# Kernel optimization log

Measured on AMD Instinct MI355X. Metric: run time of the kernel, lower is better.

## Reference

```python
import jax, jax.numpy as jnp
import numpy as np

G = 32        # group_num
PD = 8        # primary capsule dim
OC = 10       # output caps (classes)
OD = 16       # output dim
GS = 36       # group_size = primary spatial 6*6
N_ITERS = 3   # routing iterations


def conv2d(x, w, stride):
    return jax.lax.conv_general_dilated(
        x, w, window_strides=(stride, stride), padding='VALID',
        dimension_numbers=('NCHW', 'OIHW', 'NCHW'))


def squash(x):
    l2 = jnp.sum(x * x, axis=-1, keepdims=True)
    l = jnp.sqrt(l2)
    return x * (l2 / (1.0 + l2)) / (l + 1e-8)


def setup_inputs() -> dict:
    key = jax.random.key(0)
    ks = jax.random.split(key, 6)
    B = 256
    inp = jax.random.normal(ks[0], (B, 1, 28, 28), dtype=jnp.float32)
    W1 = jax.random.normal(ks[1], (256, 1, 9, 9), dtype=jnp.float32) * 0.05
    b1 = jnp.zeros((256,), dtype=jnp.float32)
    W2 = jax.random.normal(ks[2], (G * PD, 256, 9, 9), dtype=jnp.float32) * 0.01
    b2 = jnp.zeros((G * PD,), dtype=jnp.float32)
    Wcaps = jax.random.normal(ks[3], (G, GS, PD, OC * OD), dtype=jnp.float32) * 0.01
    b_route = jnp.zeros((G, 1, GS, OC), dtype=jnp.float32)
    return {'input': inp, 'W1': W1, 'b1': b1, 'W2': W2, 'b2': b2,
            'Wcaps': Wcaps, 'b_route': b_route}


def reference(input, W1, b1, W2, b2, Wcaps, b_route):
    B = input.shape[0]
    # conv1 + relu: (B,256,20,20)
    x = jax.nn.relu(conv2d(input, W1, 1) + b1[None, :, None, None])
    # primary caps conv: (B,256,6,6)
    y = conv2d(x, W2, 2) + b2[None, :, None, None]
    H = y.shape[2]
    # (B,G,PD,H,W) -> (B,G,H,W,PD) -> (B,G,GS,PD)
    y = y.reshape(B, G, PD, H, H).transpose(0, 1, 3, 4, 2).reshape(B, G, GS, PD)
    u = squash(y)
    # capsule predictions: (B,G,GS,OC,OD)
    up = jnp.einsum('bgsi,gsio->bgso', u, Wcaps).reshape(B, G, GS, OC, OD)
    # routing logits: (B,G,GS,OC)
    b = jnp.broadcast_to(jnp.transpose(b_route, (1, 0, 2, 3)), (B, G, GS, OC))
    v = None
    for r in range(N_ITERS):
        c = jax.nn.softmax(b, axis=3)                       # (B,G,GS,OC)
        s = jnp.einsum('bgso,bgsod->bgod', c, up)           # (B,G,OC,OD)
        v = squash(s)
        if r < N_ITERS - 1:
            b = b + jnp.einsum('bgsod,bgod->bgso', up, v)
    v = v.sum(axis=1)                                       # (B,OC,OD)
    probs = jnp.sqrt(jnp.sum(v * v, axis=2))                # (B,OC)
    return v, probs
```

## Files before the change

### kernel.cpp

```cpp
#include <hip/hip_runtime.h>
#include <math.h>


typedef float floatx4 __attribute__((ext_vector_type(4)));
typedef __bf16 bf16x8 __attribute__((ext_vector_type(8)));

#define XHI_OFF 0u
#define XLO_OFF 52428800u
#define WHI_OFF 104857600u
#define WLO_OFF 115867648u
#define Y2_OFF  126877696u
#define VP_OFF  136314880u
#define Y2_BYTES 9437184u

#define SL_IY   88
#define SL_IMG  1760
#define SL_PAR  7072
#define SL_TOT  14144

__device__ __forceinline__ void bf16split(float v, short& hs, short& ls) {
  unsigned u = __builtin_bit_cast(unsigned, v);
  unsigned r = (u + 0x7FFFu + ((u >> 16) & 1u)) & 0xFFFF0000u;
  hs = (short)(r >> 16);
  float lo = v - __builtin_bit_cast(float, r);
  unsigned u2 = __builtin_bit_cast(unsigned, lo);
  unsigned r2 = u2 + 0x7FFFu + ((u2 >> 16) & 1u);
  ls = (short)(r2 >> 16);
}

__global__ __launch_bounds__(320) void conv1_k(
    const float* __restrict__ inp, const float* __restrict__ W1,
    const float* __restrict__ b1, short* __restrict__ xhi,
    short* __restrict__ xlo) {
  __shared__ __align__(16) float img[784];
  __shared__ float wl[81 * 34];
  const int blk = blockIdx.x;
  const int b = blk >> 3;
  const int cbase = (blk & 7) * 32;
  const int t = threadIdx.x;

  const float4* src = (const float4*)(inp + b * 784);
  for (int idx = t; idx < 196; idx += 320) ((float4*)img)[idx] = src[idx];
  for (int idx = t; idx < 2592; idx += 320) {
    int c = idx / 81, tap = idx - c * 81;
    wl[tap * 34 + c] = W1[(cbase + c) * 81 + tap];
  }
  __syncthreads();

  const int oy = t >> 4;
  const int ct = t & 15;
  const int c0 = cbase + ct * 2;
  const float bias0 = b1[c0], bias1 = b1[c0 + 1];
  float acc0[20], acc1[20];
#pragma unroll
  for (int ox = 0; ox < 20; ox++) { acc0[ox] = bias0; acc1[ox] = bias1; }

#pragma unroll 1
  for (int i = 0; i < 9; i++) {
    float wr0[9], wr1[9];
#pragma unroll
    for (int j = 0; j < 9; j++) {
      float2 wv = *(const float2*)&wl[(i * 9 + j) * 34 + ct * 2];
      wr0[j] = wv.x; wr1[j] = wv.y;
    }
    float xr[28];
    const float4* rp = (const float4*)&img[(oy + i) * 28];
#pragma unroll
    for (int k = 0; k < 7; k++) {
      float4 v = rp[k];
      xr[4 * k] = v.x; xr[4 * k + 1] = v.y; xr[4 * k + 2] = v.z; xr[4 * k + 3] = v.w;
    }
#pragma unroll
    for (int j = 0; j < 9; j++)
#pragma unroll
      for (int ox = 0; ox < 20; ox++) {
        acc0[ox] = fmaf(xr[ox + j], wr0[j], acc0[ox]);
        acc1[ox] = fmaf(xr[ox + j], wr1[j], acc1[ox]);
      }
  }
  const long pbase = (long)(b * 400 + oy * 20) * 256 + c0;
#pragma unroll
  for (int ox = 0; ox < 20; ox++) {
    float v0 = fmaxf(acc0[ox], 0.f), v1 = fmaxf(acc1[ox], 0.f);
    short h0, l0, h1, l1;
    bf16split(v0, h0, l0);
    bf16split(v1, h1, l1);
    long a = pbase + (long)ox * 256;
    *(short2*)&xhi[a] = make_short2(h0, h1);
    *(short2*)&xlo[a] = make_short2(l0, l1);
  }
}

__global__ __launch_bounds__(256) void wtrans_k(
    const float* __restrict__ W2, short* __restrict__ whi,
    short* __restrict__ wlo) {
  const int idx = blockIdx.x * 256 + threadIdx.x;
  const int ics = idx & 7;
  const int oc = (idx >> 3) & 255;
  const int icg = (idx >> 11) & 31;
  const int tap = idx >> 16;
  short h = 0, l = 0;
  if (tap < 81) {
    const int ic = icg * 8 + ics;
    bf16split(W2[(oc * 256 + ic) * 81 + tap], h, l);
  }
  whi[idx] = h;
  wlo[idx] = l;
}

__global__ __launch_bounds__(256, 2) void conv2_k(
    const short* __restrict__ xhi, const short* __restrict__ xlo,
    const short* __restrict__ whi, const short* __restrict__ wlo,
    float* __restrict__ y2) {
  __shared__ __align__(16) short slabA[SL_TOT];

  const int blk = blockIdx.x;
  const int ks = blk & 15;
  const int mb = blk >> 4;
  const int b0 = mb * 4;
  const int t = threadIdx.x;
  const int lane = t & 63;
  const int q = lane >> 4;
  const int ln16 = lane & 15;
  const int wv = t >> 6;

  int combo[9];
#pragma unroll
  for (int mt = 0; mt < 9; mt++) {
    int row = mt * 16 + ln16;
    int im = row / 36;
    int pos = row - im * 36;
    int oy = pos / 6, ox = pos - oy * 6;
    combo[mt] = im * SL_IMG + oy * (2 * SL_IY) + ox * 8;
  }

  floatx4 acc[9][4];
#pragma unroll
  for (int mt = 0; mt < 9; mt++)
#pragma unroll
    for (int nt = 0; nt < 4; nt++) acc[mt][nt] = (floatx4)0.f;

#pragma unroll 1
  for (int icg = 0; icg < 2; icg++) {
    const int icgG = ks * 2 + icg;
    const long icoff = (long)icgG * 8;
    const long wb0 = ((long)icgG * 256 + wv * 64 + ln16) * 8 + (long)q * 65536;

    __syncthreads();
    for (int idx = t; idx < 1600; idx += 256) {
      int im = idx / 400, p = idx - im * 400;
      int iy = p / 20, ix = p - iy * 20;
      int dst = (ix & 1) * SL_PAR + im * SL_IMG + iy * SL_IY + (ix >> 1) * 8;
      *(uint4*)&slabA[dst] =
          *(const uint4*)&xhi[((long)(b0 + im) * 400 + p) * 256 + icoff];
    }
    __syncthreads();

    {
      bf16x8 cbh[4];
#pragma unroll
      for (int nt = 0; nt < 4; nt++) cbh[nt] = *(const bf16x8*)&whi[wb0 + nt * 128];
#pragma unroll 1
      for (int kst = 0; kst < 21; kst++) {
        const int t0n = (kst < 20) ? (kst + 1) * 4 : 80;
        bf16x8 nbh[4], cbl[4];
#pragma unroll
        for (int nt = 0; nt < 4; nt++) {
          nbh[nt] = *(const bf16x8*)&whi[wb0 + (long)t0n * 65536 + nt * 128];
          cbl[nt] = *(const bf16x8*)&wlo[wb0 + (long)(kst * 4) * 65536 + nt * 128];
        }
        const int tap = kst * 4 + q;
        const int i = tap / 9, j = tap - i * 9;
        const int aoff = (j & 1) * SL_PAR + i * SL_IY + (j >> 1) * 8;
#pragma unroll
        for (int bb = 0; bb < 3; bb++) {
          bf16x8 av[3];
#pragma unroll
          for (int m3 = 0; m3 < 3; m3++)
            av[m3] = *(const bf16x8*)&slabA[aoff + combo[bb * 3 + m3]];
#pragma unroll
          for (int nt = 0; nt < 4; nt++)
#pragma unroll
            for (int m3 = 0; m3 < 3; m3++)
              acc[bb * 3 + m3][nt] = __builtin_amdgcn_mfma_f32_16x16x32_bf16(
                  av[m3], cbh[nt], acc[bb * 3 + m3][nt], 0, 0, 0);
#pragma unroll
          for (int nt = 0; nt < 4; nt++)
#pragma unroll
            for (int m3 = 0; m3 < 3; m3++)
              acc[bb * 3 + m3][nt] = __builtin_amdgcn_mfma_f32_16x16x32_bf16(
                  av[m3], cbl[nt], acc[bb * 3 + m3][nt], 0, 0, 0);
        }
#pragma unroll
        for (int nt = 0; nt < 4; nt++) cbh[nt] = nbh[nt];
      }
    }

    __syncthreads();
    for (int idx = t; idx < 1600; idx += 256) {
      int im = idx / 400, p = idx - im * 400;
      int iy = p / 20, ix = p - iy * 20;
      int dst = (ix & 1) * SL_PAR + im * SL_IMG + iy * SL_IY + (ix >> 1) * 8;
      *(uint4*)&slabA[dst] =
          *(const uint4*)&xlo[((long)(b0 + im) * 400 + p) * 256 + icoff];
    }
    __syncthreads();

    {
      bf16x8 cbh[4];
#pragma unroll
      for (int nt = 0; nt < 4; nt++) cbh[nt] = *(const bf16x8*)&whi[wb0 + nt * 128];
#pragma unroll 1
      for (int kst = 0; kst < 21; kst++) {
        const int t0n = (kst < 20) ? (kst + 1) * 4 : 80;
        bf16x8 nbh[4];
#pragma unroll
        for (int nt = 0; nt < 4; nt++)
          nbh[nt] = *(const bf16x8*)&whi[wb0 + (long)t0n * 65536 + nt * 128];
        const int tap = kst * 4 + q;
        const int i = tap / 9, j = tap - i * 9;
        const int aoff = (j & 1) * SL_PAR + i * SL_IY + (j >> 1) * 8;
#pragma unroll
        for (int bb = 0; bb < 3; bb++) {
          bf16x8 av[3];
#pragma unroll
          for (int m3 = 0; m3 < 3; m3++)
            av[m3] = *(const bf16x8*)&slabA[aoff + combo[bb * 3 + m3]];
#pragma unroll
          for (int nt = 0; nt < 4; nt++)
#pragma unroll
            for (int m3 = 0; m3 < 3; m3++)
              acc[bb * 3 + m3][nt] = __builtin_amdgcn_mfma_f32_16x16x32_bf16(
                  av[m3], cbh[nt], acc[bb * 3 + m3][nt], 0, 0, 0);
        }
#pragma unroll
        for (int nt = 0; nt < 4; nt++) cbh[nt] = nbh[nt];
      }
    }
  }

#pragma unroll
  for (int mt = 0; mt < 9; mt++)
#pragma unroll
    for (int nt = 0; nt < 4; nt++) {
      int oc = wv * 64 + nt * 16 + ln16;
      int rowb = mb * 144 + mt * 16 + q * 4;
#pragma unroll
      for (int r = 0; r < 4; r++)
        atomicAdd(&y2[(long)(rowb + r) * 256 + oc], acc[mt][nt][r]);
    }
}

__global__ __launch_bounds__(256) void caps_k(
    const float* __restrict__ y2, const float* __restrict__ b2,
    const float* __restrict__ Wcaps, const float* __restrict__ b_route,
    float* __restrict__ vpart) {
  __shared__ float u[288];
  __shared__ float usc[36];
  __shared__ float up[5760];
  __shared__ float bl[360];
  __shared__ float cl[360];
  __shared__ float sv[160];
  __shared__ float vv[160];
  __shared__ float scale[10];
  const int blk = blockIdx.x;
  const int g = blk & 31, b = blk >> 5;
  const int t = threadIdx.x;

  for (int idx = t; idx < 288; idx += 256) {
    int s = idx >> 3, d = idx & 7;
    u[idx] = y2[((long)b * 36 + s) * 256 + g * 8 + d] + b2[g * 8 + d];
  }
  for (int idx = t; idx < 360; idx += 256) bl[idx] = b_route[g * 360 + idx];
  __syncthreads();
  if (t < 36) {
    float l2 = 0.f;
#pragma unroll
    for (int d = 0; d < 8; d++) { float v = u[t * 8 + d]; l2 = fmaf(v, v, l2); }
    float l = sqrtf(l2);
    usc[t] = (l2 / (1.f + l2)) / (l + 1e-8f);
  }
  __syncthreads();
  for (int idx = t; idx < 288; idx += 256) u[idx] *= usc[idx >> 3];
  __syncthreads();
  for (int idx = t; idx < 5760; idx += 256) {
    int s = idx / 160, k = idx - s * 160;
    const float* wp = Wcaps + (g * 36 + s) * 8 * 160 + k;
    float a = 0.f;
#pragma unroll
    for (int d = 0; d < 8; d++) a = fmaf(u[s * 8 + d], wp[d * 160], a);
    up[idx] = a;
  }
  __syncthreads();

  for (int r = 0; r < 3; r++) {
    if (t < 36) {
      float m = bl[t * 10];
#pragma unroll
      for (int oc = 1; oc < 10; oc++) m = fmaxf(m, bl[t * 10 + oc]);
      float e[10]; float sum = 0.f;
#pragma unroll
      for (int oc = 0; oc < 10; oc++) { e[oc] = expf(bl[t * 10 + oc] - m); sum += e[oc]; }
      float inv = 1.f / sum;
#pragma unroll
      for (int oc = 0; oc < 10; oc++) cl[t * 10 + oc] = e[oc] * inv;
    }
    __syncthreads();
    if (t < 160) {
      const int oc = t >> 4;
      float a = 0.f;
#pragma unroll 1
      for (int s = 0; s < 36; s++) a = fmaf(cl[s * 10 + oc], up[s * 160 + t], a);
      sv[t] = a;
    }
    __syncthreads();
    if (t < 10) {
      float l2 = 0.f;
#pragma unroll
      for (int od = 0; od < 16; od++) { float v = sv[t * 16 + od]; l2 = fmaf(v, v, l2); }
      scale[t] = (l2 / (1.f + l2)) / (sqrtf(l2) + 1e-8f);
    }
    __syncthreads();
    if (t < 160) vv[t] = sv[t] * scale[t >> 4];
    __syncthreads();
    if (r < 2) {
      for (int idx = t; idx < 360; idx += 256) {
        int s = idx / 10, oc = idx - s * 10;
        float a = 0.f;
#pragma unroll
        for (int od = 0; od < 16; od++)
          a = fmaf(up[s * 160 + oc * 16 + od], vv[oc * 16 + od], a);
        bl[idx] += a;
      }
      __syncthreads();
    }
  }
  if (t < 160) vpart[(b * 32 + g) * 160 + t] = vv[t];
}

__global__ __launch_bounds__(192) void final_k(
    const float* __restrict__ vpart, float* __restrict__ out) {
  __shared__ float v[160];
  const int b = blockIdx.x, t = threadIdx.x;
  if (t < 160) {
    float a = 0.f;
#pragma unroll 1
    for (int g = 0; g < 32; g++) a += vpart[(b * 32 + g) * 160 + t];
    v[t] = a;
    out[b * 160 + t] = a;
  }
  __syncthreads();
  if (t < 10) {
    float l2 = 0.f;
#pragma unroll
    for (int od = 0; od < 16; od++) { float x = v[t * 16 + od]; l2 = fmaf(x, x, l2); }
    out[40960 + b * 10 + t] = sqrtf(l2);
  }
}

extern "C" void kernel_launch(void* const* d_in, const int* in_sizes, int n_in,
                              void* d_out, int out_size, void* d_ws, size_t ws_size,
                              hipStream_t stream) {
  const float* inp     = (const float*)d_in[0];
  const float* W1      = (const float*)d_in[1];
  const float* b1      = (const float*)d_in[2];
  const float* W2      = (const float*)d_in[3];
  const float* b2      = (const float*)d_in[4];
  const float* Wcaps   = (const float*)d_in[5];
  const float* b_route = (const float*)d_in[6];
  float* out = (float*)d_out;
  char* ws = (char*)d_ws;

  short* xhi = (short*)(ws + XHI_OFF);
  short* xlo = (short*)(ws + XLO_OFF);
  short* whi = (short*)(ws + WHI_OFF);
  short* wlo = (short*)(ws + WLO_OFF);
  float* y2  = (float*)(ws + Y2_OFF);
  float* vp  = (float*)(ws + VP_OFF);

  hipMemsetAsync(y2, 0, Y2_BYTES, stream);
  conv1_k <<<2048, 320, 0, stream>>>(inp, W1, b1, xhi, xlo);
  wtrans_k<<<21504, 256, 0, stream>>>(W2, whi, wlo);
  conv2_k <<<1024, 256, 0, stream>>>(xhi, xlo, whi, wlo, y2);
  caps_k  <<<8192, 256, 0, stream>>>(y2, b2, Wcaps, b_route, vp);
  final_k <<<256, 192, 0, stream>>>(vp, out);
}
```

Measured before the change: 579.6 us.

## Fuse hi/lo conv2 passes, halve K-split, and shrink caps blocks to one wave

```diff
diff --git a/kernel.cpp b/kernel.cpp
--- a/kernel.cpp
+++ b/kernel.cpp
@@ -4,6 +4,7 @@
 
 typedef float floatx4 __attribute__((ext_vector_type(4)));
 typedef __bf16 bf16x8 __attribute__((ext_vector_type(8)));
+typedef unsigned uintx4 __attribute__((ext_vector_type(4)));
 
 #define XHI_OFF 0u
 #define XLO_OFF 52428800u
@@ -112,11 +113,12 @@
     const short* __restrict__ xhi, const short* __restrict__ xlo,
     const short* __restrict__ whi, const short* __restrict__ wlo,
     float* __restrict__ y2) {
-  __shared__ __align__(16) short slabA[SL_TOT];
+  __shared__ __align__(16) short slabH[SL_TOT];
+  __shared__ __align__(16) short slabL[SL_TOT];
 
   const int blk = blockIdx.x;
-  const int ks = blk & 15;
-  const int mb = blk >> 4;
+  const int ks = blk & 7;
+  const int mb = blk >> 3;
   const int b0 = mb * 4;
   const int t = threadIdx.x;
   const int lane = t & 63;
@@ -141,8 +143,8 @@
     for (int nt = 0; nt < 4; nt++) acc[mt][nt] = (floatx4)0.f;
 
 #pragma unroll 1
-  for (int icg = 0; icg < 2; icg++) {
-    const int icgG = ks * 2 + icg;
+  for (int icg = 0; icg < 4; icg++) {
+    const int icgG = ks * 4 + icg;
     const long icoff = (long)icgG * 8;
     const long wb0 = ((long)icgG * 256 + wv * 64 + ln16) * 8 + (long)q * 65536;
 
@@ -151,91 +153,61 @@
       int im = idx / 400, p = idx - im * 400;
       int iy = p / 20, ix = p - iy * 20;
       int dst = (ix & 1) * SL_PAR + im * SL_IMG + iy * SL_IY + (ix >> 1) * 8;
-      *(uint4*)&slabA[dst] =
-          *(const uint4*)&xhi[((long)(b0 + im) * 400 + p) * 256 + icoff];
-    }
-    __syncthreads();
-
-    {
-      bf16x8 cbh[4];
-#pragma unroll
-      for (int nt = 0; nt < 4; nt++) cbh[nt] = *(const bf16x8*)&whi[wb0 + nt * 128];
+      const long src = ((long)(b0 + im) * 400 + p) * 256 + icoff;
+      uintx4 vh = __builtin_nontemporal_load((const uintx4*)&xhi[src]);
+      uintx4 vl = __builtin_nontemporal_load((const uintx4*)&xlo[src]);
+      *(uintx4*)&slabH[dst] = vh;
+      *(uintx4*)&slabL[dst] = vl;
+    }
+    __syncthreads();
+
+    bf16x8 cbh[4], cbl[4];
+#pragma unroll
+    for (int nt = 0; nt < 4; nt++) {
+      cbh[nt] = *(const bf16x8*)&whi[wb0 + nt * 128];
+      cbl[nt] = *(const bf16x8*)&wlo[wb0 + nt * 128];
+    }
 #pragma unroll 1
-      for (int kst = 0; kst < 21; kst++) {
-        const int t0n = (kst < 20) ? (kst + 1) * 4 : 80;
-        bf16x8 nbh[4], cbl[4];
-#pragma unroll
-        for (int nt = 0; nt < 4; nt++) {
-          nbh[nt] = *(const bf16x8*)&whi[wb0 + (long)t0n * 65536 + nt * 128];
-          cbl[nt] = *(const bf16x8*)&wlo[wb0 + (long)(kst * 4) * 65536 + nt * 128];
+    for (int kst = 0; kst < 21; kst++) {
+      const int t0n = (kst < 20) ? (kst + 1) * 4 : 80;
+      bf16x8 nbh[4], nbl[4];
+#pragma unroll
+      for (int nt = 0; nt < 4; nt++) {
+        nbh[nt] = *(const bf16x8*)&whi[wb0 + (long)t0n * 65536 + nt * 128];
+        nbl[nt] = *(const bf16x8*)&wlo[wb0 + (long)t0n * 65536 + nt * 128];
+      }
+      const int tap = kst * 4 + q;
+      const int i = tap / 9, j = tap - i * 9;
+      const int aoff = (j & 1) * SL_PAR + i * SL_IY + (j >> 1) * 8;
+#pragma unroll
+      for (int bb = 0; bb < 3; bb++) {
+        bf16x8 ah[3], al[3];
+#pragma unroll
+        for (int m3 = 0; m3 < 3; m3++) {
+          ah[m3] = *(const bf16x8*)&slabH[aoff + combo[bb * 3 + m3]];
+          al[m3] = *(const bf16x8*)&slabL[aoff + combo[bb * 3 + m3]];
         }
-        const int tap = kst * 4 + q;
-        const int i = tap / 9, j = tap - i * 9;
-        const int aoff = (j & 1) * SL_PAR + i * SL_IY + (j >> 1) * 8;
-#pragma unroll
-        for (int bb = 0; bb < 3; bb++) {
-          bf16x8 av[3];
+#pragma unroll
+        for (int nt = 0; nt < 4; nt++)
 #pragma unroll
           for (int m3 = 0; m3 < 3; m3++)
-            av[m3] = *(const bf16x8*)&slabA[aoff + combo[bb * 3 + m3]];
-#pragma unroll
-          for (int nt = 0; nt < 4; nt++)
-#pragma unroll
-            for (int m3 = 0; m3 < 3; m3++)
-              acc[bb * 3 + m3][nt] = __builtin_amdgcn_mfma_f32_16x16x32_bf16(
-                  av[m3], cbh[nt], acc[bb * 3 + m3][nt], 0, 0, 0);
-#pragma unroll
-          for (int nt = 0; nt < 4; nt++)
-#pragma unroll
-            for (int m3 = 0; m3 < 3; m3++)
-              acc[bb * 3 + m3][nt] = __builtin_amdgcn_mfma_f32_16x16x32_bf16(
-                  av[m3], cbl[nt], acc[bb * 3 + m3][nt], 0, 0, 0);
-        }
-#pragma unroll
-        for (int nt = 0; nt < 4; nt++) cbh[nt] = nbh[nt];
+            acc[bb * 3 + m3][nt] = __builtin_amdgcn_mfma_f32_16x16x32_bf16(
+                ah[m3], cbh[nt], acc[bb * 3 + m3][nt], 0, 0, 0);
+#pragma unroll
+        for (int nt = 0; nt < 4; nt++)
+#pragma unroll
+          for (int m3 = 0; m3 < 3; m3++)
+            acc[bb * 3 + m3][nt] = __builtin_amdgcn_mfma_f32_16x16x32_bf16(
+                ah[m3], cbl[nt], acc[bb * 3 + m3][nt], 0, 0, 0);
+#pragma unroll
+        for (int nt = 0; nt < 4; nt++)
+#pragma unroll
+          for (int m3 = 0; m3 < 3; m3++)
+            acc[bb * 3 + m3][nt] = __builtin_amdgcn_mfma_f32_16x16x32_bf16(
+                al[m3], cbh[nt], acc[bb * 3 + m3][nt], 0, 0, 0);
       }
-    }
-
-    __syncthreads();
-    for (int idx = t; idx < 1600; idx += 256) {
-      int im = idx / 400, p = idx - im * 400;
-      int iy = p / 20, ix = p - iy * 20;
-      int dst = (ix & 1) * SL_PAR + im * SL_IMG + iy * SL_IY + (ix >> 1) * 8;
-      *(uint4*)&slabA[dst] =
-          *(const uint4*)&xlo[((long)(b0 + im) * 400 + p) * 256 + icoff];
-    }
-    __syncthreads();
-
-    {
-      bf16x8 cbh[4];
-#pragma unroll
-      for (int nt = 0; nt < 4; nt++) cbh[nt] = *(const bf16x8*)&whi[wb0 + nt * 128];
-#pragma unroll 1
-      for (int kst = 0; kst < 21; kst++) {
-        const int t0n = (kst < 20) ? (kst + 1) * 4 : 80;
-        bf16x8 nbh[4];
-#pragma unroll
-        for (int nt = 0; nt < 4; nt++)
-          nbh[nt] = *(const bf16x8*)&whi[wb0 + (long)t0n * 65536 + nt * 128];
-        const int tap = kst * 4 + q;
-        const int i = tap / 9, j = tap - i * 9;
-        const int aoff = (j & 1) * SL_PAR + i * SL_IY + (j >> 1) * 8;
-#pragma unroll
-        for (int bb = 0; bb < 3; bb++) {
-          bf16x8 av[3];
-#pragma unroll
-          for (int m3 = 0; m3 < 3; m3++)
-            av[m3] = *(const bf16x8*)&slabA[aoff + combo[bb * 3 + m3]];
-#pragma unroll
-          for (int nt = 0; nt < 4; nt++)
-#pragma unroll
-            for (int m3 = 0; m3 < 3; m3++)
-              acc[bb * 3 + m3][nt] = __builtin_amdgcn_mfma_f32_16x16x32_bf16(
-                  av[m3], cbh[nt], acc[bb * 3 + m3][nt], 0, 0, 0);
-        }
-#pragma unroll
-        for (int nt = 0; nt < 4; nt++) cbh[nt] = nbh[nt];
-      }
+#pragma unroll
+      for (int nt = 0; nt < 4; nt++) { cbh[nt] = nbh[nt]; cbl[nt] = nbl[nt]; }
     }
   }
 
@@ -251,7 +223,7 @@
     }
 }
 
-__global__ __launch_bounds__(256) void caps_k(
+__global__ __launch_bounds__(64) void caps_k(
     const float* __restrict__ y2, const float* __restrict__ b2,
     const float* __restrict__ Wcaps, const float* __restrict__ b_route,
     float* __restrict__ vpart) {
@@ -267,11 +239,11 @@
   const int g = blk & 31, b = blk >> 5;
   const int t = threadIdx.x;
 
-  for (int idx = t; idx < 288; idx += 256) {
+  for (int idx = t; idx < 288; idx += 64) {
     int s = idx >> 3, d = idx & 7;
     u[idx] = y2[((long)b * 36 + s) * 256 + g * 8 + d] + b2[g * 8 + d];
   }
-  for (int idx = t; idx < 360; idx += 256) bl[idx] = b_route[g * 360 + idx];
+  for (int idx = t; idx < 360; idx += 64) bl[idx] = b_route[g * 360 + idx];
   __syncthreads();
   if (t < 36) {
     float l2 = 0.f;
@@ -281,9 +253,9 @@
     usc[t] = (l2 / (1.f + l2)) / (l + 1e-8f);
   }
   __syncthreads();
-  for (int idx = t; idx < 288; idx += 256) u[idx] *= usc[idx >> 3];
-  __syncthreads();
-  for (int idx = t; idx < 5760; idx += 256) {
+  for (int idx = t; idx < 288; idx += 64) u[idx] *= usc[idx >> 3];
+  __syncthreads();
+  for (int idx = t; idx < 5760; idx += 64) {
     int s = idx / 160, k = idx - s * 160;
     const float* wp = Wcaps + (g * 36 + s) * 8 * 160 + k;
     float a = 0.f;
@@ -306,12 +278,12 @@
       for (int oc = 0; oc < 10; oc++) cl[t * 10 + oc] = e[oc] * inv;
     }
     __syncthreads();
-    if (t < 160) {
-      const int oc = t >> 4;
+    for (int idx = t; idx < 160; idx += 64) {
+      const int oc = idx >> 4;
       float a = 0.f;
-#pragma unroll 1
-      for (int s = 0; s < 36; s++) a = fmaf(cl[s * 10 + oc], up[s * 160 + t], a);
-      sv[t] = a;
+#pragma unroll 4
+      for (int s = 0; s < 36; s++) a = fmaf(cl[s * 10 + oc], up[s * 160 + idx], a);
+      sv[idx] = a;
     }
     __syncthreads();
     if (t < 10) {
@@ -321,10 +293,10 @@
       scale[t] = (l2 / (1.f + l2)) / (sqrtf(l2) + 1e-8f);
     }
     __syncthreads();
-    if (t < 160) vv[t] = sv[t] * scale[t >> 4];
+    for (int idx = t; idx < 160; idx += 64) vv[idx] = sv[idx] * scale[idx >> 4];
     __syncthreads();
     if (r < 2) {
-      for (int idx = t; idx < 360; idx += 256) {
+      for (int idx = t; idx < 360; idx += 64) {
         int s = idx / 10, oc = idx - s * 10;
         float a = 0.f;
 #pragma unroll
@@ -335,7 +307,7 @@
       __syncthreads();
     }
   }
-  if (t < 160) vpart[(b * 32 + g) * 160 + t] = vv[t];
+  for (int idx = t; idx < 160; idx += 64) vpart[(b * 32 + g) * 160 + idx] = vv[idx];
 }
 
 __global__ __launch_bounds__(192) void final_k(
@@ -344,7 +316,7 @@
   const int b = blockIdx.x, t = threadIdx.x;
   if (t < 160) {
     float a = 0.f;
-#pragma unroll 1
+#pragma unroll 4
     for (int g = 0; g < 32; g++) a += vpart[(b * 32 + g) * 160 + t];
     v[t] = a;
     out[b * 160 + t] = a;
@@ -378,10 +350,10 @@
   float* y2  = (float*)(ws + Y2_OFF);
   float* vp  = (float*)(ws + VP_OFF);
 
-  hipMemsetAsync(y2, 0, Y2_BYTES, stream);
+  (void)hipMemsetAsync(y2, 0, Y2_BYTES, stream);
   conv1_k <<<2048, 320, 0, stream>>>(inp, W1, b1, xhi, xlo);
   wtrans_k<<<21504, 256, 0, stream>>>(W2, whi, wlo);
-  conv2_k <<<1024, 256, 0, stream>>>(xhi, xlo, whi, wlo, y2);
-  caps_k  <<<8192, 256, 0, stream>>>(y2, b2, Wcaps, b_route, vp);
+  conv2_k <<<512, 256, 0, stream>>>(xhi, xlo, whi, wlo, y2);
+  caps_k  <<<8192, 64, 0, stream>>>(y2, b2, Wcaps, b_route, vp);
   final_k <<<256, 192, 0, stream>>>(vp, out);
 }
```

Result: slower. 616.6 us (+6.4%).

## Tile weight transpose through LDS, halve conv2 split-K, use nontemporal loads

Applied to the files above, without the earlier changes.

```diff
diff --git a/kernel.cpp b/kernel.cpp
--- a/kernel.cpp
+++ b/kernel.cpp
@@ -4,19 +4,22 @@
 
 typedef float floatx4 __attribute__((ext_vector_type(4)));
 typedef __bf16 bf16x8 __attribute__((ext_vector_type(8)));
+typedef unsigned uintx4 __attribute__((ext_vector_type(4)));
 
 #define XHI_OFF 0u
 #define XLO_OFF 52428800u
 #define WHI_OFF 104857600u
-#define WLO_OFF 115867648u
-#define Y2_OFF  126877696u
-#define VP_OFF  136314880u
+#define WLO_OFF 116391936u
+#define Y2_OFF  127926272u
+#define VP_OFF  137363456u
 #define Y2_BYTES 9437184u
 
 #define SL_IY   88
 #define SL_IMG  1760
 #define SL_PAR  7072
 #define SL_TOT  14144
+
+#define TAPSTRIDE 65536
 
 __device__ __forceinline__ void bf16split(float v, short& hs, short& ls) {
   unsigned u = __builtin_bit_cast(unsigned, v);
@@ -94,18 +97,30 @@
 __global__ __launch_bounds__(256) void wtrans_k(
     const float* __restrict__ W2, short* __restrict__ whi,
     short* __restrict__ wlo) {
-  const int idx = blockIdx.x * 256 + threadIdx.x;
-  const int ics = idx & 7;
-  const int oc = (idx >> 3) & 255;
-  const int icg = (idx >> 11) & 31;
-  const int tap = idx >> 16;
-  short h = 0, l = 0;
-  if (tap < 81) {
-    const int ic = icg * 8 + ics;
-    bf16split(W2[(oc * 256 + ic) * 81 + tap], h, l);
-  }
-  whi[idx] = h;
-  wlo[idx] = l;
+  __shared__ short lh[81 * 258];
+  __shared__ short ll[81 * 258];
+  const int blk = blockIdx.x;
+  const int icg = blk & 31, ocg = blk >> 5;
+  const int t = threadIdx.x;
+
+  for (int idx = t; idx < 20736; idx += 256) {
+    int c = idx / 648, r = idx - c * 648;
+    int ics = r / 81, tap = r - ics * 81;
+    float v = W2[(long)(ocg * 32 + c) * 20736 + icg * 648 + r];
+    short h, l;
+    bf16split(v, h, l);
+    lh[tap * 258 + c * 8 + ics] = h;
+    ll[tap * 258 + c * 8 + ics] = l;
+  }
+  __syncthreads();
+  const long obase = (long)icg * 2048 + ocg * 256 + t;
+#pragma unroll 1
+  for (int tap = 0; tap < 88; tap++) {
+    short h = 0, l = 0;
+    if (tap < 81) { h = lh[tap * 258 + t]; l = ll[tap * 258 + t]; }
+    whi[obase + (long)tap * TAPSTRIDE] = h;
+    wlo[obase + (long)tap * TAPSTRIDE] = l;
+  }
 }
 
 __global__ __launch_bounds__(256, 2) void conv2_k(
@@ -115,8 +130,8 @@
   __shared__ __align__(16) short slabA[SL_TOT];
 
   const int blk = blockIdx.x;
-  const int ks = blk & 15;
-  const int mb = blk >> 4;
+  const int ks = blk & 7;
+  const int mb = blk >> 3;
   const int b0 = mb * 4;
   const int t = threadIdx.x;
   const int lane = t & 63;
@@ -141,18 +156,19 @@
     for (int nt = 0; nt < 4; nt++) acc[mt][nt] = (floatx4)0.f;
 
 #pragma unroll 1
-  for (int icg = 0; icg < 2; icg++) {
-    const int icgG = ks * 2 + icg;
+  for (int icg = 0; icg < 4; icg++) {
+    const int icgG = ks * 4 + icg;
     const long icoff = (long)icgG * 8;
-    const long wb0 = ((long)icgG * 256 + wv * 64 + ln16) * 8 + (long)q * 65536;
+    const long wb0 = ((long)icgG * 256 + wv * 64 + ln16) * 8 + (long)q * TAPSTRIDE;
 
     __syncthreads();
     for (int idx = t; idx < 1600; idx += 256) {
       int im = idx / 400, p = idx - im * 400;
       int iy = p / 20, ix = p - iy * 20;
       int dst = (ix & 1) * SL_PAR + im * SL_IMG + iy * SL_IY + (ix >> 1) * 8;
-      *(uint4*)&slabA[dst] =
-          *(const uint4*)&xhi[((long)(b0 + im) * 400 + p) * 256 + icoff];
+      const long src = ((long)(b0 + im) * 400 + p) * 256 + icoff;
+      uintx4 vh = __builtin_nontemporal_load((const uintx4*)&xhi[src]);
+      *(uintx4*)&slabA[dst] = vh;
     }
     __syncthreads();
 
@@ -166,8 +182,8 @@
         bf16x8 nbh[4], cbl[4];
 #pragma unroll
         for (int nt = 0; nt < 4; nt++) {
-          nbh[nt] = *(const bf16x8*)&whi[wb0 + (long)t0n * 65536 + nt * 128];
-          cbl[nt] = *(const bf16x8*)&wlo[wb0 + (long)(kst * 4) * 65536 + nt * 128];
+          nbh[nt] = *(const bf16x8*)&whi[wb0 + (long)t0n * TAPSTRIDE + nt * 128];
+          cbl[nt] = *(const bf16x8*)&wlo[wb0 + (long)(kst * 4) * TAPSTRIDE + nt * 128];
         }
         const int tap = kst * 4 + q;
         const int i = tap / 9, j = tap - i * 9;
@@ -201,8 +217,9 @@
       int im = idx / 400, p = idx - im * 400;
       int iy = p / 20, ix = p - iy * 20;
       int dst = (ix & 1) * SL_PAR + im * SL_IMG + iy * SL_IY + (ix >> 1) * 8;
-      *(uint4*)&slabA[dst] =
-          *(const uint4*)&xlo[((long)(b0 + im) * 400 + p) * 256 + icoff];
+      const long src = ((long)(b0 + im) * 400 + p) * 256 + icoff;
+      uintx4 vl = __builtin_nontemporal_load((const uintx4*)&xlo[src]);
+      *(uintx4*)&slabA[dst] = vl;
     }
     __syncthreads();
 
@@ -216,7 +233,7 @@
         bf16x8 nbh[4];
 #pragma unroll
         for (int nt = 0; nt < 4; nt++)
-          nbh[nt] = *(const bf16x8*)&whi[wb0 + (long)t0n * 65536 + nt * 128];
+          nbh[nt] = *(const bf16x8*)&whi[wb0 + (long)t0n * TAPSTRIDE + nt * 128];
         const int tap = kst * 4 + q;
         const int i = tap / 9, j = tap - i * 9;
         const int aoff = (j & 1) * SL_PAR + i * SL_IY + (j >> 1) * 8;
@@ -344,7 +361,7 @@
   const int b = blockIdx.x, t = threadIdx.x;
   if (t < 160) {
     float a = 0.f;
-#pragma unroll 1
+#pragma unroll 4
     for (int g = 0; g < 32; g++) a += vpart[(b * 32 + g) * 160 + t];
     v[t] = a;
     out[b * 160 + t] = a;
@@ -378,10 +395,10 @@
   float* y2  = (float*)(ws + Y2_OFF);
   float* vp  = (float*)(ws + VP_OFF);
 
-  hipMemsetAsync(y2, 0, Y2_BYTES, stream);
+  (void)hipMemsetAsync(y2, 0, Y2_BYTES, stream);
   conv1_k <<<2048, 320, 0, stream>>>(inp, W1, b1, xhi, xlo);
-  wtrans_k<<<21504, 256, 0, stream>>>(W2, whi, wlo);
-  conv2_k <<<1024, 256, 0, stream>>>(xhi, xlo, whi, wlo, y2);
+  wtrans_k<<<256, 256, 0, stream>>>(W2, whi, wlo);
+  conv2_k <<<512, 256, 0, stream>>>(xhi, xlo, whi, wlo, y2);
   caps_k  <<<8192, 256, 0, stream>>>(y2, b2, Wcaps, b_route, vp);
   final_k <<<256, 192, 0, stream>>>(vp, out);
 }
```

New measurement: 561.4 us. 3.1% less time.
